# Performance work log

Hardware: AMD Instinct MI355X
Metric: run time of the kernel (lower is better)

The kernel has to match this reference:

```python
import jax, jax.numpy as jnp
import numpy as np

B, N, F_IN, F_HID, F_OUT = 16, 1024, 512, 512, 512


def setup_inputs() -> dict:
    key = jax.random.key(0)
    ks = jax.random.split(key, 8)
    return {
        "batch_graph": jax.random.normal(ks[0], (B, N, F_IN), dtype=jnp.float32),
        "adj": jax.random.uniform(ks[1], (B, N, N), dtype=jnp.float32),
        "W1": jax.random.normal(ks[2], (F_IN, F_HID), dtype=jnp.float32) * (1.0 / np.sqrt(F_IN)),
        "b1": jax.random.normal(ks[3], (F_HID,), dtype=jnp.float32) * 0.02,
        "W2": jax.random.normal(ks[4], (F_HID, F_HID), dtype=jnp.float32) * (1.0 / np.sqrt(F_HID)),
        "b2": jax.random.normal(ks[5], (F_HID,), dtype=jnp.float32) * 0.02,
        "W3": jax.random.normal(ks[6], (F_HID, F_OUT), dtype=jnp.float32) * (1.0 / np.sqrt(F_HID)),
        "b3": jax.random.normal(ks[7], (F_OUT,), dtype=jnp.float32) * 0.02,
    }


def _normalize_adj(adj):
    # torch: adj.sum(1) sums over rows -> per-column sums, shape [B, N]
    colsum = jnp.sum(adj, axis=1)
    r = jnp.where(colsum > 0, colsum ** -0.5, 0.0)  # inf -> 0 as in original
    # (adj @ diag(r)).T @ diag(r)  ==  r[:,None] * adj^T * r[None,:]  (per batch)
    return r[:, :, None] * jnp.swapaxes(adj, 1, 2) * r[:, None, :]


def reference(batch_graph, adj, W1, b1, W2, b2, W3, b3):
    # The original builds a dense (B*N)x(B*N) block-diagonal adjacency; the
    # block-diagonal matmul is mathematically a per-graph batched matmul.
    # Dropout is identity in eval mode.
    a = _normalize_adj(adj)  # [B, N, N]

    def layer(x, W, b):
        return jnp.einsum('bij,bjf->bif', a, x @ W) + b

    x = jax.nn.relu(layer(batch_graph, W1, b1))
    x = jax.nn.relu(layer(x, W2, b2))
    return layer(x, W3, b3)  # [B, N, F_OUT]
```

## Files before the change

### kernel.cpp

```cpp
#include <hip/hip_runtime.h>
#include <hip/hip_bf16.h>

typedef __bf16 bf16;
typedef __bf16 bf16x4 __attribute__((ext_vector_type(4)));
typedef __bf16 bf16x8 __attribute__((ext_vector_type(8)));
typedef float f32x4 __attribute__((ext_vector_type(4)));

#define B_ 16
#define N_ 1024
#define F_ 512

__device__ __forceinline__ float rdv(const void* p, size_t i, int f32) {
  return f32 ? ((const float*)p)[i] : (float)((const bf16*)p)[i];
}

__device__ __forceinline__ void gld16(const bf16* g, bf16* l) {
  __builtin_amdgcn_global_load_lds(
      (const __attribute__((address_space(1))) unsigned int*)g,
      (__attribute__((address_space(3))) unsigned int*)l, 16, 0, 0);
}

__global__ void k_pre(const void* b1, const void* b2, const void* b3,
                      const void* W1, const void* W2, const void* W3,
                      const void* X, const void* adj,
                      int* __restrict__ flag, float* __restrict__ bc,
                      bf16* __restrict__ Wt, bf16* __restrict__ xc,
                      bf16* __restrict__ adjT, float* __restrict__ csp) {
  __shared__ float tile[64][65];
  __shared__ float red2[4][64];
  __shared__ int fred[4];
  const int bid = blockIdx.x;
  const int t = threadIdx.x;

  {
    const unsigned* w = (const unsigned*)W1;
    int c = 0;
#pragma unroll
    for (int i = 0; i < 8; ++i) c += (((w[t + 256 * i] >> 7) & 0xFFu) >= 130u) ? 1 : 0;
#pragma unroll
    for (int o = 32; o > 0; o >>= 1) c += __shfl_down(c, o);
    if ((t & 63) == 0) fred[t >> 6] = c;
  }
  __syncthreads();
  const int f = (fred[0] + fred[1] + fred[2] + fred[3]) > 512;
  if (bid == 0 && t == 0) flag[0] = f;

  if (bid < 6) {
    const int j = bid * 256 + t;
    const void* src = (j < 512) ? b1 : (j < 1024 ? b2 : b3);
    bc[j] = rdv(src, (size_t)(j & 511), f);
  } else if (bid < 774) {
    float(*wt32)[65] = tile;
    const int bid2 = bid - 6;
    const int z = bid2 >> 8, ti = bid2 & 255;
    const int f0 = (ti & 15) * 32, k0 = (ti >> 4) * 32;
    const int tx = t & 31, ty = t >> 5;
    const void* W = (z == 0) ? W1 : ((z == 1) ? W2 : W3);
    bf16* dst = Wt + (size_t)z * F_ * F_;
#pragma unroll
    for (int s = 0; s < 4; ++s)
      wt32[ty + 8 * s][tx] = rdv(W, (size_t)(k0 + ty + 8 * s) * F_ + f0 + tx, f);
    __syncthreads();
#pragma unroll
    for (int s = 0; s < 4; ++s)
      dst[(size_t)(f0 + ty + 8 * s) * F_ + k0 + tx] = (bf16)wt32[tx][ty + 8 * s];
  } else if (bid < 8966) {
    const size_t i4 = ((size_t)(bid - 774) * 256 + t) * 4;
    if (f) {
      f32x4 v = *(const f32x4*)((const float*)X + i4);
      bf16 o[4] = {(bf16)v[0], (bf16)v[1], (bf16)v[2], (bf16)v[3]};
      *(ulong1*)&xc[i4] = *(ulong1*)o;
    } else {
      *(ulong1*)&xc[i4] = *(const ulong1*)((const bf16*)X + i4);
    }
  } else {
    const int bid2 = bid - 8966;
    const int tx = t & 15, ty = t >> 4;
    const int b = bid2 >> 8;
    const int i0 = ((bid2 >> 4) & 15) * 64, j0 = (bid2 & 15) * 64;
    const size_t sb = (size_t)b * N_ * N_;
    if (f) {
      const float* src = (const float*)adj + sb;
#pragma unroll
      for (int s = 0; s < 4; ++s) {
        const int jj = ty + 16 * s;
        f32x4 v = *(const f32x4*)&src[(size_t)(j0 + jj) * N_ + i0 + 4 * tx];
#pragma unroll
        for (int u = 0; u < 4; ++u) tile[jj][4 * tx + u] = v[u];
      }
    } else {
      const bf16* src = (const bf16*)adj + sb;
#pragma unroll
      for (int s = 0; s < 4; ++s) {
        const int jj = ty + 16 * s;
        bf16x4 v = *(const bf16x4*)&src[(size_t)(j0 + jj) * N_ + i0 + 4 * tx];
#pragma unroll
        for (int u = 0; u < 4; ++u) tile[jj][4 * tx + u] = (float)v[u];
      }
    }
    __syncthreads();
    {
      const int cc = t & 63, g = t >> 6;
      float s = 0.f;
#pragma unroll
      for (int r = 0; r < 16; ++r) s += tile[g * 16 + r][cc];
      red2[g][cc] = s;
    }
    bf16* dst = adjT + sb;
#pragma unroll
    for (int s = 0; s < 4; ++s) {
      const int ii = ty + 16 * s;
      bf16x4 o;
#pragma unroll
      for (int u = 0; u < 4; ++u) o[u] = (bf16)tile[4 * tx + u][ii];
      *(bf16x4*)&dst[(size_t)(i0 + ii) * N_ + j0 + 4 * tx] = o;
    }
    __syncthreads();
    if (t < 64)
      csp[((size_t)(j0 >> 6) * B_ + b) * N_ + i0 + t] =
          red2[0][t] + red2[1][t] + red2[2][t] + red2[3][t];
  }
}

__device__ __forceinline__ float rscale(const float* __restrict__ csp, int b, int node) {
  float c = 0.f;
#pragma unroll
  for (int z = 0; z < 16; ++z) c += csp[((size_t)z * B_ + b) * N_ + node];
  return c > 0.f ? rsqrtf(c) : 0.f;
}

template <int BIAS, int RELU, int OUTDYN, int SCALEN, int SCALEM, int GX>
__global__ __launch_bounds__(256)
void k_gemm_bt(const bf16* __restrict__ A, const bf16* __restrict__ Bt,
               const float* __restrict__ bias, void* __restrict__ C,
               const int* __restrict__ flag, const float* __restrict__ csp,
               int Nc, int K, long sA, long sB, long sC) {
  __shared__ __align__(16) char smem[65536];
  const int id = blockIdx.x;
  const int xcd = id & 7, p = id >> 3;
  const int bz = xcd * 2 + (p >> 5);
  const int tl = p & 31;
  const int bx = tl % GX, by = tl / GX;

  const int tid = threadIdx.x;
  const int wid = tid >> 6, lane = tid & 63;
  const int wm = wid >> 1, wn = wid & 1;
  const int quad = lane >> 4, l16 = lane & 15;
  const int rl = lane >> 3;
  const int cg8 = ((lane & 7) ^ rl) * 8;
  const int h = l16 & 7;

  const bf16* gA = A + (size_t)bz * sA + (size_t)by * 128 * K;
  const bf16* gB = Bt + (size_t)bz * sB + (size_t)bx * 128 * K;

  f32x4 acc[4][4];
#pragma unroll
  for (int i = 0; i < 4; ++i)
#pragma unroll
    for (int j = 0; j < 4; ++j) acc[i][j] = (f32x4){0.f, 0.f, 0.f, 0.f};

  auto stage = [&](int d, int k0) {
    bf16* As = (bf16*)(smem + d * 32768);
    bf16* Bs = (bf16*)(smem + d * 32768 + 16384);
#pragma unroll
    for (int i = 0; i < 4; ++i) {
      const int r0 = wid * 32 + i * 8;
      gld16(gA + (size_t)(r0 + rl) * K + k0 + cg8, &As[r0 * 64]);
      gld16(gB + (size_t)(r0 + rl) * K + k0 + cg8, &Bs[r0 * 64]);
    }
  };

  stage(0, 0);
  for (int k0 = 0; k0 < K; k0 += 64) {
    const int cur = (k0 >> 6) & 1;
    if (k0 + 64 < K) {
      stage(1 - cur, k0 + 64);
      asm volatile("s_waitcnt vmcnt(8)\n\ts_barrier" ::: "memory");
    } else {
      asm volatile("s_waitcnt vmcnt(0)\n\ts_barrier" ::: "memory");
    }
    const bf16* As = (const bf16*)(smem + cur * 32768);
    const bf16* Bs = (const bf16*)(smem + cur * 32768 + 16384);
#pragma unroll
    for (int s = 0; s < 2; ++s) {
      bf16x8 af[4], bfv[4];
#pragma unroll
      for (int tm = 0; tm < 4; ++tm)
        af[tm] = *(const bf16x8*)&As[(wm * 64 + tm * 16 + l16) * 64 +
                                     (((quad + 4 * s) ^ h) * 8)];
#pragma unroll
      for (int tn = 0; tn < 4; ++tn)
        bfv[tn] = *(const bf16x8*)&Bs[(wn * 64 + tn * 16 + l16) * 64 +
                                      (((quad + 4 * s) ^ h) * 8)];
#pragma unroll
      for (int tm = 0; tm < 4; ++tm)
#pragma unroll
        for (int tn = 0; tn < 4; ++tn)
          acc[tm][tn] =
              __builtin_amdgcn_mfma_f32_16x16x32_bf16(af[tm], bfv[tn], acc[tm][tn], 0, 0, 0);
    }
    asm volatile("s_barrier" ::: "memory");
  }

  float* rsh = (float*)(smem + 37376);
  if (SCALEN || SCALEM) {
    if (tid < 128) {
      const int node = (SCALEM ? by * 128 : bx * 128) + tid;
      rsh[tid] = rscale(csp, bz, node);
    }
    __syncthreads();
  }

  const size_t cb = (size_t)bz * sC;
  const int mb_w = by * 128 + wm * 64;
  const int nb_w = bx * 128 + wn * 64;

  if (OUTDYN) {
    const int of32 = flag[0];
#pragma unroll
    for (int tn = 0; tn < 4; ++tn) {
      const int n = nb_w + tn * 16 + l16;
      float bv = BIAS ? bias[n] : 0.f;
      const float cscale = SCALEN ? rsh[wn * 64 + tn * 16 + l16] : 1.f;
#pragma unroll
      for (int tm = 0; tm < 4; ++tm) {
        const int m0 = mb_w + tm * 16 + quad * 4;
#pragma unroll
        for (int r = 0; r < 4; ++r) {
          float v = acc[tm][tn][r];
          if (SCALEM) v *= rsh[wm * 64 + tm * 16 + quad * 4 + r];
          if (SCALEN) v *= cscale;
          v += bv;
          if (RELU) v = v > 0.f ? v : 0.f;
          const size_t idx = cb + (size_t)(m0 + r) * Nc + n;
          if (of32) ((float*)C)[idx] = v;
          else      ((bf16*)C)[idx] = (bf16)v;
        }
      }
    }
  } else {
    bf16* W = (bf16*)smem + wid * (64 * 72);
#pragma unroll
    for (int tn = 0; tn < 4; ++tn) {
      const int n = nb_w + tn * 16 + l16;
      float bv = BIAS ? bias[n] : 0.f;
      const float cscale = SCALEN ? rsh[wn * 64 + tn * 16 + l16] : 1.f;
#pragma unroll
      for (int tm = 0; tm < 4; ++tm) {
#pragma unroll
        for (int r = 0; r < 4; ++r) {
          float v = acc[tm][tn][r];
          if (SCALEM) v *= rsh[wm * 64 + tm * 16 + quad * 4 + r];
          if (SCALEN) v *= cscale;
          v += bv;
          if (RELU) v = v > 0.f ? v : 0.f;
          W[(tm * 16 + quad * 4 + r) * 72 + tn * 16 + l16] = (bf16)v;
        }
      }
    }
    bf16* gC = (bf16*)C + cb;
#pragma unroll
    for (int i = 0; i < 8; ++i) {
      const int row = i * 8 + rl;
      bf16x8 v = *(const bf16x8*)&W[row * 72 + (lane & 7) * 8];
      *(bf16x8*)&gC[(size_t)(mb_w + row) * Nc + nb_w + (lane & 7) * 8] = v;
    }
  }
}

extern "C" void kernel_launch(void* const* d_in, const int* in_sizes, int n_in,
                              void* d_out, int out_size, void* d_ws, size_t ws_size,
                              hipStream_t stream) {
  char* ws = (char*)d_ws;
  float* csp  = (float*)ws;
  int*  flag  = (int*)(ws + 1048576);
  float* bc   = (float*)(ws + 1048832);
  bf16* adjT  = (bf16*)(ws + 1056768);
  bf16* Wt    = (bf16*)(ws + 1056768 + 33554432);
  bf16* Zt    = (bf16*)(ws + 1056768 + 33554432 + 3 * F_ * F_ * 2);
  bf16* Xc = (bf16*)d_out;

  const long sW = 0;
  const long sX = (long)N_ * F_;
  const long sZ = (long)F_ * N_;
  const long sAn = (long)N_ * N_;

  k_pre<<<6 + 768 + 8192 + 4096, 256, 0, stream>>>(
      d_in[3], d_in[5], d_in[7], d_in[2], d_in[4], d_in[6], d_in[0], d_in[1],
      flag, bc, Wt, Xc, adjT, csp);

  k_gemm_bt<0, 0, 0, 1, 0, 8><<<512, 256, 0, stream>>>(Wt,               Xc, nullptr,   Zt, flag, csp, N_, F_, sW, sX, sZ);
  k_gemm_bt<1, 1, 0, 0, 1, 4><<<512, 256, 0, stream>>>(adjT,             Zt, bc,        Xc, flag, csp, F_, N_, sAn, sZ, sX);
  k_gemm_bt<0, 0, 0, 1, 0, 8><<<512, 256, 0, stream>>>(Wt + F_ * F_,     Xc, nullptr,   Zt, flag, csp, N_, F_, sW, sX, sZ);
  k_gemm_bt<1, 1, 0, 0, 1, 4><<<512, 256, 0, stream>>>(adjT,             Zt, bc + 512,  Xc, flag, csp, F_, N_, sAn, sZ, sX);
  k_gemm_bt<0, 0, 0, 1, 0, 8><<<512, 256, 0, stream>>>(Wt + 2 * F_ * F_, Xc, nullptr,   Zt, flag, csp, N_, F_, sW, sX, sZ);
  k_gemm_bt<1, 0, 1, 0, 1, 4><<<512, 256, 0, stream>>>(adjT,             Zt, bc + 1024, d_out, flag, csp, F_, N_, sAn, sZ, sX);
}
```

Baseline: 265.6 us.

## Restructure preprocessing: larger adj transpose tiles, interleaved blocks, wave-local dtype probe

Result: faster. 259.3 us (-2.4%).

```diff
diff --git a/kernel.cpp b/kernel.cpp
--- a/kernel.cpp
+++ b/kernel.cpp
@@ -26,32 +26,88 @@
                       int* __restrict__ flag, float* __restrict__ bc,
                       bf16* __restrict__ Wt, bf16* __restrict__ xc,
                       bf16* __restrict__ adjT, float* __restrict__ csp) {
-  __shared__ float tile[64][65];
+  __shared__ float tile[128][65];
   __shared__ float red2[4][64];
-  __shared__ int fred[4];
   const int bid = blockIdx.x;
   const int t = threadIdx.x;
 
+  int f;
   {
     const unsigned* w = (const unsigned*)W1;
+    const int l = t & 63;
     int c = 0;
 #pragma unroll
-    for (int i = 0; i < 8; ++i) c += (((w[t + 256 * i] >> 7) & 0xFFu) >= 130u) ? 1 : 0;
-#pragma unroll
-    for (int o = 32; o > 0; o >>= 1) c += __shfl_down(c, o);
-    if ((t & 63) == 0) fred[t >> 6] = c;
-  }
-  __syncthreads();
-  const int f = (fred[0] + fred[1] + fred[2] + fred[3]) > 512;
-  if (bid == 0 && t == 0) flag[0] = f;
-
-  if (bid < 6) {
-    const int j = bid * 256 + t;
-    const void* src = (j < 512) ? b1 : (j < 1024 ? b2 : b3);
-    bc[j] = rdv(src, (size_t)(j & 511), f);
-  } else if (bid < 774) {
-    float(*wt32)[65] = tile;
-    const int bid2 = bid - 6;
+    for (int i = 0; i < 4; ++i) {
+      unsigned v = w[l + 64 * i];
+      c += __popcll(__ballot(((v >> 7) & 0xFFu) >= 130u));
+    }
+    f = c > 64;
+  }
+
+  if (bid < 6144) {
+    const int q = bid / 3, r = bid - 3 * q;
+    if (r == 0) {
+      const int b = q >> 7, rem = q & 127;
+      const int j0 = (rem >> 4) << 7, i0 = (rem & 15) << 6;
+      const size_t sb = (size_t)b * N_ * N_;
+      const int tx = t & 15, jr = t >> 4;
+      if (f) {
+        const float* src = (const float*)adj + sb;
+#pragma unroll
+        for (int s = 0; s < 8; ++s) {
+          const int jj = jr + 16 * s;
+          f32x4 v = *(const f32x4*)&src[(size_t)(j0 + jj) * N_ + i0 + 4 * tx];
+#pragma unroll
+          for (int u = 0; u < 4; ++u) tile[jj][4 * tx + u] = v[u];
+        }
+      } else {
+        const bf16* src = (const bf16*)adj + sb;
+#pragma unroll
+        for (int s = 0; s < 8; ++s) {
+          const int jj = jr + 16 * s;
+          bf16x4 v = *(const bf16x4*)&src[(size_t)(j0 + jj) * N_ + i0 + 4 * tx];
+#pragma unroll
+          for (int u = 0; u < 4; ++u) tile[jj][4 * tx + u] = (float)v[u];
+        }
+      }
+      __syncthreads();
+      {
+        const int cc = t & 63, g = t >> 6;
+        float s = 0.f;
+#pragma unroll
+        for (int rr = 0; rr < 32; ++rr) s += tile[g * 32 + rr][cc];
+        red2[g][cc] = s;
+      }
+      bf16* dst = adjT + sb;
+      const int oct = t & 15;
+#pragma unroll
+      for (int s = 0; s < 4; ++s) {
+        const int ii = (t >> 4) + 16 * s;
+        bf16x8 o;
+#pragma unroll
+        for (int u = 0; u < 8; ++u) o[u] = (bf16)tile[8 * oct + u][ii];
+        *(bf16x8*)&dst[(size_t)(i0 + ii) * N_ + j0 + 8 * oct] = o;
+      }
+      __syncthreads();
+      if (t < 64)
+        csp[((size_t)(j0 >> 7) * B_ + b) * N_ + i0 + t] =
+            red2[0][t] + red2[1][t] + red2[2][t] + red2[3][t];
+    } else {
+      const int c = 2 * q + (r - 1);
+      const size_t i8 = ((size_t)c * 256 + t) * 8;
+      if (f) {
+        const float* xf = (const float*)X + i8;
+        f32x4 v0 = *(const f32x4*)xf;
+        f32x4 v1 = *(const f32x4*)(xf + 4);
+        bf16x8 o = {(bf16)v0[0], (bf16)v0[1], (bf16)v0[2], (bf16)v0[3],
+                    (bf16)v1[0], (bf16)v1[1], (bf16)v1[2], (bf16)v1[3]};
+        *(bf16x8*)&xc[i8] = o;
+      } else {
+        *(f32x4*)&xc[i8] = *(const f32x4*)((const bf16*)X + i8);
+      }
+    }
+  } else if (bid < 6912) {
+    const int bid2 = bid - 6144;
     const int z = bid2 >> 8, ti = bid2 & 255;
     const int f0 = (ti & 15) * 32, k0 = (ti >> 4) * 32;
     const int tx = t & 31, ty = t >> 5;
@@ -59,73 +115,23 @@
     bf16* dst = Wt + (size_t)z * F_ * F_;
 #pragma unroll
     for (int s = 0; s < 4; ++s)
-      wt32[ty + 8 * s][tx] = rdv(W, (size_t)(k0 + ty + 8 * s) * F_ + f0 + tx, f);
+      tile[ty + 8 * s][tx] = rdv(W, (size_t)(k0 + ty + 8 * s) * F_ + f0 + tx, f);
     __syncthreads();
 #pragma unroll
     for (int s = 0; s < 4; ++s)
-      dst[(size_t)(f0 + ty + 8 * s) * F_ + k0 + tx] = (bf16)wt32[tx][ty + 8 * s];
-  } else if (bid < 8966) {
-    const size_t i4 = ((size_t)(bid - 774) * 256 + t) * 4;
-    if (f) {
-      f32x4 v = *(const f32x4*)((const float*)X + i4);
-      bf16 o[4] = {(bf16)v[0], (bf16)v[1], (bf16)v[2], (bf16)v[3]};
-      *(ulong1*)&xc[i4] = *(ulong1*)o;
-    } else {
-      *(ulong1*)&xc[i4] = *(const ulong1*)((const bf16*)X + i4);
-    }
+      dst[(size_t)(f0 + ty + 8 * s) * F_ + k0 + tx] = (bf16)tile[tx][ty + 8 * s];
   } else {
-    const int bid2 = bid - 8966;
-    const int tx = t & 15, ty = t >> 4;
-    const int b = bid2 >> 8;
-    const int i0 = ((bid2 >> 4) & 15) * 64, j0 = (bid2 & 15) * 64;
-    const size_t sb = (size_t)b * N_ * N_;
-    if (f) {
-      const float* src = (const float*)adj + sb;
-#pragma unroll
-      for (int s = 0; s < 4; ++s) {
-        const int jj = ty + 16 * s;
-        f32x4 v = *(const f32x4*)&src[(size_t)(j0 + jj) * N_ + i0 + 4 * tx];
-#pragma unroll
-        for (int u = 0; u < 4; ++u) tile[jj][4 * tx + u] = v[u];
-      }
-    } else {
-      const bf16* src = (const bf16*)adj + sb;
-#pragma unroll
-      for (int s = 0; s < 4; ++s) {
-        const int jj = ty + 16 * s;
-        bf16x4 v = *(const bf16x4*)&src[(size_t)(j0 + jj) * N_ + i0 + 4 * tx];
-#pragma unroll
-        for (int u = 0; u < 4; ++u) tile[jj][4 * tx + u] = (float)v[u];
-      }
-    }
-    __syncthreads();
-    {
-      const int cc = t & 63, g = t >> 6;
-      float s = 0.f;
-#pragma unroll
-      for (int r = 0; r < 16; ++r) s += tile[g * 16 + r][cc];
-      red2[g][cc] = s;
-    }
-    bf16* dst = adjT + sb;
-#pragma unroll
-    for (int s = 0; s < 4; ++s) {
-      const int ii = ty + 16 * s;
-      bf16x4 o;
-#pragma unroll
-      for (int u = 0; u < 4; ++u) o[u] = (bf16)tile[4 * tx + u][ii];
-      *(bf16x4*)&dst[(size_t)(i0 + ii) * N_ + j0 + 4 * tx] = o;
-    }
-    __syncthreads();
-    if (t < 64)
-      csp[((size_t)(j0 >> 6) * B_ + b) * N_ + i0 + t] =
-          red2[0][t] + red2[1][t] + red2[2][t] + red2[3][t];
+    const int j = (bid - 6912) * 256 + t;
+    const void* src = (j < 512) ? b1 : (j < 1024 ? b2 : b3);
+    bc[j] = rdv(src, (size_t)(j & 511), f);
+    if (bid == 6912 && t == 0) flag[0] = f;
   }
 }
 
 __device__ __forceinline__ float rscale(const float* __restrict__ csp, int b, int node) {
   float c = 0.f;
 #pragma unroll
-  for (int z = 0; z < 16; ++z) c += csp[((size_t)z * B_ + b) * N_ + node];
+  for (int z = 0; z < 8; ++z) c += csp[((size_t)z * B_ + b) * N_ + node];
   return c > 0.f ? rsqrtf(c) : 0.f;
 }
 
@@ -285,7 +291,7 @@
   const long sZ = (long)F_ * N_;
   const long sAn = (long)N_ * N_;
 
-  k_pre<<<6 + 768 + 8192 + 4096, 256, 0, stream>>>(
+  k_pre<<<6144 + 768 + 6, 256, 0, stream>>>(
       d_in[3], d_in[5], d_in[7], d_in[2], d_in[4], d_in[6], d_in[0], d_in[1],
       flag, bc, Wt, Xc, adjT, csp);
 
```
